# Performance work log

Hardware: AMD Instinct MI355X
Metric: run time of the kernel (lower is better)

Reference implementation:

```python
import jax, jax.numpy as jnp
import numpy as np

E4M3_MAX = 448.0
MARGIN_FACTOR = 2.0  # margin=1 -> 2**1


def _fp8_scale(t):
    amax = jnp.max(jnp.abs(t))
    scale = E4M3_MAX / (amax * MARGIN_FACTOR + 1e-12)
    return jnp.clip(scale, 1e-12, 1e12)


def _quantize_e4m3_sim(t, scale):
    # simulated E4M3: clamp then round to 1/8 grid (module's non-native fallback)
    s = jnp.clip(t * scale, -E4M3_MAX, E4M3_MAX)
    return jnp.round(s * 8.0) / 8.0


def setup_inputs() -> dict:
    key = jax.random.key(0)
    k1, k2 = jax.random.split(key)
    M, IN, OUT = 32768, 1024, 1024
    x = jax.random.normal(k1, (M, IN), dtype=jnp.float32)
    weight_master = jax.random.normal(k2, (OUT, IN), dtype=jnp.float32) * (1.0 / np.sqrt(IN))
    bias = jnp.zeros((OUT,), dtype=jnp.float32)
    return {"x": x, "weight_master": weight_master, "bias": bias}


def reference(x, weight_master, bias):
    # weight quantization (done at init / sync_weights)
    w_scale = _fp8_scale(weight_master)
    w_fp8 = _quantize_e4m3_sim(weight_master, w_scale)
    # per-call dynamic activation scale + quantize
    a_scale = _fp8_scale(x)
    x_fp8 = _quantize_e4m3_sim(x, a_scale)
    # dequantize and GEMM (fp8_forward_dequant path)
    x_deq = x_fp8 / a_scale
    w_deq = w_fp8 / w_scale
    out = jnp.einsum('mk,nk->mn', x_deq, w_deq) + bias
    return out
```

## Files before the change

kernel.cpp:

```cpp
#include <hip/hip_runtime.h>
#include <hip/hip_bf16.h>
#include <hip/hip_fp16.h>

typedef _Float16 half8 __attribute__((ext_vector_type(8)));
typedef float f32x4 __attribute__((ext_vector_type(4)));

#define GM 32768
#define GN 1024
#define GK 1024
#define BM 128
#define BN 128
#define BK 32

#define AX_BLOCKS 1024
#define AW_BLOCKS 32
#define QX_BLOCKS 16384
#define QW_BLOCKS 512

__device__ __forceinline__ float fp8_scale_from_amax(float amax) {
    float s = 448.0f / (amax * 2.0f + 1e-12f);
    return fminf(fmaxf(s, 1e-12f), 1e12f);
}

__global__ __launch_bounds__(256) void amax_kernel(const float4* __restrict__ x,
                                                   const float4* __restrict__ w,
                                                   unsigned* __restrict__ amax_bits,
                                                   int nx4, int nw4) {
    int b = blockIdx.x;
    const float4* src; int n4; unsigned* slot; int nb; int bl;
    if (b < AX_BLOCKS) { src = x; n4 = nx4; slot = amax_bits + 0; nb = AX_BLOCKS; bl = b; }
    else               { src = w; n4 = nw4; slot = amax_bits + 1; nb = AW_BLOCKS; bl = b - AX_BLOCKS; }
    float m = 0.0f;
    int stride = nb * 256;
    for (int i = bl * 256 + threadIdx.x; i < n4; i += stride) {
        float4 v = src[i];
        m = fmaxf(m, fabsf(v.x)); m = fmaxf(m, fabsf(v.y));
        m = fmaxf(m, fabsf(v.z)); m = fmaxf(m, fabsf(v.w));
    }
    #pragma unroll
    for (int off = 32; off; off >>= 1) m = fmaxf(m, __shfl_xor(m, off));
    if ((threadIdx.x & 63) == 0) atomicMax(slot, __float_as_uint(m));
}

__global__ __launch_bounds__(256) void quant_kernel(const float* __restrict__ x,
                                                    const float* __restrict__ w,
                                                    _Float16* __restrict__ X8,
                                                    _Float16* __restrict__ W8,
                                                    const unsigned* __restrict__ amax_bits) {
    int b = blockIdx.x;
    const float* src; _Float16* dst; int bl; int slot;
    if (b < QX_BLOCKS) { src = x; dst = X8; bl = b; slot = 0; }
    else               { src = w; dst = W8; bl = b - QX_BLOCKS; slot = 1; }
    float amax  = __uint_as_float(amax_bits[slot]);
    float scale = fp8_scale_from_amax(amax);
    size_t base = ((size_t)bl * 256 + threadIdx.x) * 8;
    float4 v0 = *(const float4*)(src + base);
    float4 v1 = *(const float4*)(src + base + 4);
    float vs[8] = {v0.x, v0.y, v0.z, v0.w, v1.x, v1.y, v1.z, v1.w};
    half8 h;
    #pragma unroll
    for (int j = 0; j < 8; ++j) {
        float s = vs[j] * scale;
        s = fminf(fmaxf(s, -448.0f), 448.0f);
        h[j] = (_Float16)rintf(s * 8.0f);
    }
    *(half8*)(dst + base) = h;
}

__global__ __launch_bounds__(256) void gemm_kernel(const _Float16* __restrict__ A,
                                                   const _Float16* __restrict__ B,
                                                   const float* __restrict__ bias,
                                                   float* __restrict__ C,
                                                   const unsigned* __restrict__ amax_bits) {
    __shared__ _Float16 As[BM * BK];
    __shared__ _Float16 Bs[BN * BK];

    const int tid  = threadIdx.x;
    const int wid  = tid >> 6;
    const int lane = tid & 63;
    const int wr   = wid >> 1, wc = wid & 1;

    const int bid = blockIdx.x;
    const int swz = (bid & 7) * 256 + (bid >> 3);
    const int bn  = swz & 7;
    const int bm  = swz >> 3;
    const int row0 = bm * BM, col0 = bn * BN;

    f32x4 acc[4][4] = {};

    const int srow = tid >> 2;
    const int scol = (tid & 3) * 8;
    const _Float16* gA = A + (size_t)(row0 + srow) * GK + scol;
    const _Float16* gB = B + (size_t)(col0 + srow) * GK + scol;

    char* ldsA = (char*)As + wid * 1024;
    char* ldsB = (char*)Bs + wid * 1024;

    const int l16 = lane & 15;
    const int kcb = (lane >> 4) * 16;

    for (int kt = 0; kt < GK; kt += BK) {
        __builtin_amdgcn_global_load_lds(
            (const __attribute__((address_space(1))) void*)(gA + kt),
            (__attribute__((address_space(3))) void*)(ldsA), 16, 0, 0);
        __builtin_amdgcn_global_load_lds(
            (const __attribute__((address_space(1))) void*)(gA + kt + (size_t)64 * GK),
            (__attribute__((address_space(3))) void*)(ldsA + 4096), 16, 0, 0);
        __builtin_amdgcn_global_load_lds(
            (const __attribute__((address_space(1))) void*)(gB + kt),
            (__attribute__((address_space(3))) void*)(ldsB), 16, 0, 0);
        __builtin_amdgcn_global_load_lds(
            (const __attribute__((address_space(1))) void*)(gB + kt + (size_t)64 * GK),
            (__attribute__((address_space(3))) void*)(ldsB + 4096), 16, 0, 0);
        __syncthreads();

        half8 af[4], bf[4];
        #pragma unroll
        for (int mi = 0; mi < 4; ++mi) {
            int r = wr * 64 + mi * 16 + l16;
            af[mi] = *(const half8*)((const char*)As + r * 64 + kcb);
        }
        #pragma unroll
        for (int ni = 0; ni < 4; ++ni) {
            int r = wc * 64 + ni * 16 + l16;
            bf[ni] = *(const half8*)((const char*)Bs + r * 64 + kcb);
        }
        #pragma unroll
        for (int mi = 0; mi < 4; ++mi)
            #pragma unroll
            for (int ni = 0; ni < 4; ++ni)
                acc[mi][ni] = __builtin_amdgcn_mfma_f32_16x16x32_f16(af[mi], bf[ni], acc[mi][ni], 0, 0, 0);
        __syncthreads();
    }

    float sa = fp8_scale_from_amax(__uint_as_float(amax_bits[0]));
    float sw = fp8_scale_from_amax(__uint_as_float(amax_bits[1]));
    float r  = 1.0f / (64.0f * sa * sw);

    const int orow = row0 + wr * 64 + (lane >> 4) * 4;
    const int ocol = col0 + wc * 64 + l16;
    #pragma unroll
    for (int mi = 0; mi < 4; ++mi) {
        #pragma unroll
        for (int ni = 0; ni < 4; ++ni) {
            int cc = ocol + ni * 16;
            float bv = bias[cc];
            #pragma unroll
            for (int i = 0; i < 4; ++i) {
                int rr = orow + mi * 16 + i;
                C[(size_t)rr * GN + cc] = acc[mi][ni][i] * r + bv;
            }
        }
    }
}

extern "C" void kernel_launch(void* const* d_in, const int* in_sizes, int n_in,
                              void* d_out, int out_size, void* d_ws, size_t ws_size,
                              hipStream_t stream) {
    const float* x    = (const float*)d_in[0];
    const float* w    = (const float*)d_in[1];
    const float* bias = (const float*)d_in[2];
    float* out        = (float*)d_out;

    unsigned* amax_bits = (unsigned*)d_ws;
    _Float16* X8 = (_Float16*)((char*)d_ws + 256);
    _Float16* W8 = (_Float16*)((char*)d_ws + 256 + (size_t)GM * GK * 2);

    hipMemsetAsync(d_ws, 0, 8, stream);

    amax_kernel<<<AX_BLOCKS + AW_BLOCKS, 256, 0, stream>>>(
        (const float4*)x, (const float4*)w, amax_bits, GM * GK / 4, GN * GK / 4);

    quant_kernel<<<QX_BLOCKS + QW_BLOCKS, 256, 0, stream>>>(x, w, X8, W8, amax_bits);

    gemm_kernel<<<(GM / BM) * (GN / BN), 256, 0, stream>>>(X8, W8, bias, out, amax_bits);
}
```

Baseline: 378.3 us.

## Use 256x256 GEMM tiles with triple-buffered swizzled LDS and unrolled amax

The GEMM moves to 256x256 tiles with 512 threads and a three-slot LDS ring filled by direct global-to-LDS loads two stages ahead. It uses explicit vmcnt waits with a single barrier per k-step, XOR-swizzled LDS layout to avoid bank conflicts, and s_setprio around the MFMA bursts. This aims to hide load latency and raise data reuse per tile. The amax reduction is also fully unrolled with independent accumulators and a fixed trip count that relies on the exact problem sizes. Costs include 96KB of LDS and 128 accumulator registers per thread, and only 512 blocks across the device.

New measurement: 381.2 us. Within noise of the previous version (+0.8%).

```diff
diff --git a/kernel.cpp b/kernel.cpp
--- a/kernel.cpp
+++ b/kernel.cpp
@@ -8,12 +8,18 @@
 #define GM 32768
 #define GN 1024
 #define GK 1024
-#define BM 128
-#define BN 128
+
+#define BM 256
+#define BN 256
 #define BK 32
-
-#define AX_BLOCKS 1024
-#define AW_BLOCKS 32
+#define NT (GK / BK)
+#define SLOT_BYTES 32768
+#define B_OFF 16384
+#define A_HALF 8192
+#define LDS_BYTES (3 * SLOT_BYTES)
+
+#define AX_BLOCKS 2048
+#define AW_BLOCKS 64
 #define QX_BLOCKS 16384
 #define QW_BLOCKS 512
 
@@ -24,19 +30,27 @@
 
 __global__ __launch_bounds__(256) void amax_kernel(const float4* __restrict__ x,
                                                    const float4* __restrict__ w,
-                                                   unsigned* __restrict__ amax_bits,
-                                                   int nx4, int nw4) {
+                                                   unsigned* __restrict__ amax_bits) {
     int b = blockIdx.x;
-    const float4* src; int n4; unsigned* slot; int nb; int bl;
-    if (b < AX_BLOCKS) { src = x; n4 = nx4; slot = amax_bits + 0; nb = AX_BLOCKS; bl = b; }
-    else               { src = w; n4 = nw4; slot = amax_bits + 1; nb = AW_BLOCKS; bl = b - AX_BLOCKS; }
-    float m = 0.0f;
-    int stride = nb * 256;
-    for (int i = bl * 256 + threadIdx.x; i < n4; i += stride) {
-        float4 v = src[i];
-        m = fmaxf(m, fabsf(v.x)); m = fmaxf(m, fabsf(v.y));
-        m = fmaxf(m, fabsf(v.z)); m = fmaxf(m, fabsf(v.w));
-    }
+    const float4* src; unsigned* slot; int nb, bl;
+    if (b < AX_BLOCKS) { src = x; slot = amax_bits + 0; nb = AX_BLOCKS; bl = b; }
+    else               { src = w; slot = amax_bits + 1; nb = AW_BLOCKS; bl = b - AX_BLOCKS; }
+    const size_t stride = (size_t)nb * 256;
+    const float4* p = src + (size_t)bl * 256 + threadIdx.x;
+    float m0 = 0.f, m1 = 0.f, m2 = 0.f, m3 = 0.f;
+    #pragma unroll
+    for (int j = 0; j < 4; ++j) {
+        float4 a = p[0];
+        float4 c = p[stride];
+        float4 d = p[2 * stride];
+        float4 e = p[3 * stride];
+        p += 4 * stride;
+        m0 = fmaxf(m0, fmaxf(fmaxf(fabsf(a.x), fabsf(a.y)), fmaxf(fabsf(a.z), fabsf(a.w))));
+        m1 = fmaxf(m1, fmaxf(fmaxf(fabsf(c.x), fabsf(c.y)), fmaxf(fabsf(c.z), fabsf(c.w))));
+        m2 = fmaxf(m2, fmaxf(fmaxf(fabsf(d.x), fabsf(d.y)), fmaxf(fabsf(d.z), fabsf(d.w))));
+        m3 = fmaxf(m3, fmaxf(fmaxf(fabsf(e.x), fabsf(e.y)), fmaxf(fabsf(e.z), fabsf(e.w))));
+    }
+    float m = fmaxf(fmaxf(m0, m1), fmaxf(m2, m3));
     #pragma unroll
     for (int off = 32; off; off >>= 1) m = fmaxf(m, __shfl_xor(m, off));
     if ((threadIdx.x & 63) == 0) atomicMax(slot, __float_as_uint(m));
@@ -67,88 +81,119 @@
     *(half8*)(dst + base) = h;
 }
 
-__global__ __launch_bounds__(256) void gemm_kernel(const _Float16* __restrict__ A,
-                                                   const _Float16* __restrict__ B,
-                                                   const float* __restrict__ bias,
-                                                   float* __restrict__ C,
-                                                   const unsigned* __restrict__ amax_bits) {
-    __shared__ _Float16 As[BM * BK];
-    __shared__ _Float16 Bs[BN * BK];
+__global__ __launch_bounds__(512, 2) void gemm_kernel(const _Float16* __restrict__ A,
+                                                      const _Float16* __restrict__ B,
+                                                      const float* __restrict__ bias,
+                                                      float* __restrict__ C,
+                                                      const unsigned* __restrict__ amax_bits) {
+    extern __shared__ char lds[];
 
     const int tid  = threadIdx.x;
     const int wid  = tid >> 6;
     const int lane = tid & 63;
-    const int wr   = wid >> 1, wc = wid & 1;
+    const int wr   = wid >> 2;
+    const int wc   = wid & 3;
+    const int l16  = lane & 15;
+    const int kq   = lane >> 4;
 
     const int bid = blockIdx.x;
-    const int swz = (bid & 7) * 256 + (bid >> 3);
-    const int bn  = swz & 7;
-    const int bm  = swz >> 3;
+    const int swz = (bid & 7) * 64 + (bid >> 3);
+    const int bm  = swz >> 2;
+    const int bn  = swz & 3;
     const int row0 = bm * BM, col0 = bn * BN;
 
-    f32x4 acc[4][4] = {};
-
-    const int srow = tid >> 2;
-    const int scol = (tid & 3) * 8;
-    const _Float16* gA = A + (size_t)(row0 + srow) * GK + scol;
-    const _Float16* gB = B + (size_t)(col0 + srow) * GK + scol;
-
-    char* ldsA = (char*)As + wid * 1024;
-    char* ldsB = (char*)Bs + wid * 1024;
-
-    const int l16 = lane & 15;
-    const int kcb = (lane >> 4) * 16;
-
-    for (int kt = 0; kt < GK; kt += BK) {
-        __builtin_amdgcn_global_load_lds(
-            (const __attribute__((address_space(1))) void*)(gA + kt),
-            (__attribute__((address_space(3))) void*)(ldsA), 16, 0, 0);
-        __builtin_amdgcn_global_load_lds(
-            (const __attribute__((address_space(1))) void*)(gA + kt + (size_t)64 * GK),
-            (__attribute__((address_space(3))) void*)(ldsA + 4096), 16, 0, 0);
-        __builtin_amdgcn_global_load_lds(
-            (const __attribute__((address_space(1))) void*)(gB + kt),
-            (__attribute__((address_space(3))) void*)(ldsB), 16, 0, 0);
-        __builtin_amdgcn_global_load_lds(
-            (const __attribute__((address_space(1))) void*)(gB + kt + (size_t)64 * GK),
-            (__attribute__((address_space(3))) void*)(ldsB + 4096), 16, 0, 0);
-        __syncthreads();
-
-        half8 af[4], bf[4];
-        #pragma unroll
-        for (int mi = 0; mi < 4; ++mi) {
-            int r = wr * 64 + mi * 16 + l16;
-            af[mi] = *(const half8*)((const char*)As + r * 64 + kcb);
-        }
-        #pragma unroll
-        for (int ni = 0; ni < 4; ++ni) {
-            int r = wc * 64 + ni * 16 + l16;
-            bf[ni] = *(const half8*)((const char*)Bs + r * 64 + kcb);
-        }
-        #pragma unroll
-        for (int mi = 0; mi < 4; ++mi)
-            #pragma unroll
-            for (int ni = 0; ni < 4; ++ni)
-                acc[mi][ni] = __builtin_amdgcn_mfma_f32_16x16x32_f16(af[mi], bf[ni], acc[mi][ni], 0, 0, 0);
-        __syncthreads();
-    }
+    const int rho  = tid >> 2;
+    const int kap  = tid & 3;
+    const int coff = ((kap ^ ((rho >> 1) & 3)) << 3);
+    const _Float16* sA0 = A + (size_t)(row0 + rho) * GK + coff;
+    const _Float16* sA1 = A + (size_t)(row0 + 128 + rho) * GK + coff;
+    const _Float16* sB0 = B + (size_t)(col0 + rho) * GK + coff;
+    const _Float16* sB1 = B + (size_t)(col0 + 128 + rho) * GK + coff;
+    const int dA0 = wid * 1024;
+    const int dA1 = A_HALF + wid * 1024;
+    const int dB0 = B_OFF + wid * 1024;
+    const int dB1 = B_OFF + A_HALF + wid * 1024;
+
+    const int rsw  = kq ^ ((l16 >> 1) & 3);
+    const int offA = (wr * 128 + l16) * 64 + (rsw << 4);
+    const int offB = B_OFF + (wc * 64 + l16) * 64 + (rsw << 4);
+
+    f32x4 acc[8][4] = {};
+
+#define STAGE(slotidx) do {                                                            \
+    char* sb_ = lds + (slotidx) * SLOT_BYTES;                                          \
+    __builtin_amdgcn_global_load_lds((const __attribute__((address_space(1))) void*)sA0, \
+        (__attribute__((address_space(3))) void*)(sb_ + dA0), 16, 0, 0);               \
+    __builtin_amdgcn_global_load_lds((const __attribute__((address_space(1))) void*)sA1, \
+        (__attribute__((address_space(3))) void*)(sb_ + dA1), 16, 0, 0);               \
+    __builtin_amdgcn_global_load_lds((const __attribute__((address_space(1))) void*)sB0, \
+        (__attribute__((address_space(3))) void*)(sb_ + dB0), 16, 0, 0);               \
+    __builtin_amdgcn_global_load_lds((const __attribute__((address_space(1))) void*)sB1, \
+        (__attribute__((address_space(3))) void*)(sb_ + dB1), 16, 0, 0);               \
+    sA0 += BK; sA1 += BK; sB0 += BK; sB1 += BK;                                        \
+} while (0)
+
+#define MM(f, av)                                                                  \
+    acc[f][0] = __builtin_amdgcn_mfma_f32_16x16x32_f16(av, bf0, acc[f][0], 0, 0, 0); \
+    acc[f][1] = __builtin_amdgcn_mfma_f32_16x16x32_f16(av, bf1, acc[f][1], 0, 0, 0); \
+    acc[f][2] = __builtin_amdgcn_mfma_f32_16x16x32_f16(av, bf2, acc[f][2], 0, 0, 0); \
+    acc[f][3] = __builtin_amdgcn_mfma_f32_16x16x32_f16(av, bf3, acc[f][3], 0, 0, 0);
+
+#define COMPUTE(slotidx) do {                                  \
+    const char* cb_ = lds + (slotidx) * SLOT_BYTES;            \
+    half8 bf0 = *(const half8*)(cb_ + offB + 0 * 1024);        \
+    half8 bf1 = *(const half8*)(cb_ + offB + 1 * 1024);        \
+    half8 bf2 = *(const half8*)(cb_ + offB + 2 * 1024);        \
+    half8 bf3 = *(const half8*)(cb_ + offB + 3 * 1024);        \
+    half8 a0 = *(const half8*)(cb_ + offA + 0 * 1024);         \
+    half8 a1 = *(const half8*)(cb_ + offA + 1 * 1024);         \
+    half8 a2 = *(const half8*)(cb_ + offA + 2 * 1024);         \
+    half8 a3 = *(const half8*)(cb_ + offA + 3 * 1024);         \
+    __builtin_amdgcn_s_setprio(1);                             \
+    MM(0, a0) MM(1, a1) MM(2, a2) MM(3, a3)                    \
+    __builtin_amdgcn_s_setprio(0);                             \
+    half8 a4 = *(const half8*)(cb_ + offA + 4 * 1024);         \
+    half8 a5 = *(const half8*)(cb_ + offA + 5 * 1024);         \
+    half8 a6 = *(const half8*)(cb_ + offA + 6 * 1024);         \
+    half8 a7 = *(const half8*)(cb_ + offA + 7 * 1024);         \
+    __builtin_amdgcn_s_setprio(1);                             \
+    MM(4, a4) MM(5, a5) MM(6, a6) MM(7, a7)                    \
+    __builtin_amdgcn_s_setprio(0);                             \
+} while (0)
+
+    STAGE(0);
+    STAGE(1);
+    for (int t = 0; t < NT; ++t) {
+        if (t < NT - 1) { asm volatile("s_waitcnt vmcnt(4)" ::: "memory"); }
+        else            { asm volatile("s_waitcnt vmcnt(0)" ::: "memory"); }
+        __builtin_amdgcn_s_barrier();
+        asm volatile("" ::: "memory");
+        if (t + 2 < NT) STAGE((t + 2) % 3);
+        COMPUTE(t % 3);
+    }
+
+#undef STAGE
+#undef COMPUTE
+#undef MM
 
     float sa = fp8_scale_from_amax(__uint_as_float(amax_bits[0]));
     float sw = fp8_scale_from_amax(__uint_as_float(amax_bits[1]));
-    float r  = 1.0f / (64.0f * sa * sw);
-
-    const int orow = row0 + wr * 64 + (lane >> 4) * 4;
+    float rs = 1.0f / (64.0f * sa * sw);
+
+    const int orow = row0 + wr * 128 + kq * 4;
     const int ocol = col0 + wc * 64 + l16;
-    #pragma unroll
-    for (int mi = 0; mi < 4; ++mi) {
+    float bvv[4];
+    #pragma unroll
+    for (int n = 0; n < 4; ++n) bvv[n] = bias[ocol + n * 16];
+    #pragma unroll
+    for (int f = 0; f < 8; ++f) {
         #pragma unroll
-        for (int ni = 0; ni < 4; ++ni) {
-            int cc = ocol + ni * 16;
-            float bv = bias[cc];
+        for (int n = 0; n < 4; ++n) {
+            const int cc = ocol + n * 16;
             #pragma unroll
             for (int i = 0; i < 4; ++i) {
-                int rr = orow + mi * 16 + i;
-                C[(size_t)rr * GN + cc] = acc[mi][ni][i] * r + bv;
+                const int rr = orow + f * 16 + i;
+                C[(size_t)rr * GN + cc] = acc[f][n][i] * rs + bvv[n];
             }
         }
     }
@@ -169,9 +214,11 @@
     hipMemsetAsync(d_ws, 0, 8, stream);
 
     amax_kernel<<<AX_BLOCKS + AW_BLOCKS, 256, 0, stream>>>(
-        (const float4*)x, (const float4*)w, amax_bits, GM * GK / 4, GN * GK / 4);
+        (const float4*)x, (const float4*)w, amax_bits);
 
     quant_kernel<<<QX_BLOCKS + QW_BLOCKS, 256, 0, stream>>>(x, w, X8, W8, amax_bits);
 
-    gemm_kernel<<<(GM / BM) * (GN / BN), 256, 0, stream>>>(X8, W8, bias, out, amax_bits);
-}
+    (void)hipFuncSetAttribute((const void*)gemm_kernel,
+                              hipFuncAttributeMaxDynamicSharedMemorySize, LDS_BYTES);
+    gemm_kernel<<<(GM / BM) * (GN / BN), 512, LDS_BYTES, stream>>>(X8, W8, bias, out, amax_bits);
+}
```
